# Kernel tuning notes

Hardware: AMD Instinct MI355X
Metric: run time of the kernel (lower is better)

## Reference

```python
import jax, jax.numpy as jnp
import numpy as np

N_CLASSES = 16
REG = 0.1


def setup_inputs() -> dict:
    key = jax.random.key(0)
    k1, k2, k3, k4 = jax.random.split(key, 4)
    N, M, d = 4096, 4096, 1024
    X = jax.random.normal(k1, (N, d), dtype=jnp.float32)
    y = jax.random.randint(k2, (N,), 0, N_CLASSES)
    Xq = jax.random.normal(k3, (M, d), dtype=jnp.float32)
    m = 0.01 * jax.random.normal(k4, (1, d), dtype=jnp.float32)
    kappa = jnp.asarray(0.1, dtype=jnp.float32)
    nu = jnp.asarray(float(d), dtype=jnp.float32)
    triu_diag = jnp.ones((d,), dtype=jnp.float32)
    triu_lower = jnp.eye(d, dtype=jnp.float32) + 0.01 * jax.random.normal(
        jax.random.fold_in(key, 7), (d, d), dtype=jnp.float32)
    return {"X": X, "y": y, "Xq": Xq, "m": m, "kappa": kappa, "nu": nu,
            "triu_diag": triu_diag, "triu_lower": triu_lower}


def reference(X, y, Xq, m, kappa, nu, triu_diag, triu_lower):
    d = X.shape[1]
    C = N_CLASSES
    # Cholesky-factor prior scale: diag(|triu_diag|) + strictly-lower part of triu_lower
    strict_lower = jnp.tril(jnp.ones((d, d), dtype=X.dtype), -1)
    L = jnp.diag(jnp.abs(triu_diag)) + triu_lower * strict_lower
    kap = jnp.abs(kappa) + 1e-6
    nu_ = jnp.maximum(nu, d - 1 + 1e-6)

    # --- fit (vectorized over classes) ---
    onehot = jax.nn.one_hot(y, C, dtype=X.dtype)          # [N, C]
    Nj = onehot.sum(axis=0)                               # [C]
    sums = onehot.T @ X                                   # [C, d] grouped sums
    means = sums / Nj[:, None]                            # [C, d]
    mu = (kap / (kap + Nj))[:, None] * m + (Nj / (kap + Nj))[:, None] * means  # [C, d]
    # grouped scatter: S[c] = X_c^T X_c, via class-weighted features
    Xw = X[:, None, :] * onehot[:, :, None]               # [N, C, d]
    S = jnp.einsum('ncd,ne->cde', Xw, X)                  # [C, d, d]
    base = L @ L.T + kap * (m.T @ m)                      # [d, d]
    sigma = (base[None] + S
             - (kap + Nj)[:, None, None] * jnp.einsum('cd,ce->cde', mu, mu))
    sigma = sigma / (nu_ + Nj + d + 2)[:, None, None]     # [C, d, d]
    eye = jnp.eye(d, dtype=X.dtype)
    sigma_inv = (1.0 - REG) * jnp.linalg.inv(sigma) + REG * eye[None]

    # --- predict: negative Mahalanobis quadratic form per (query, class) ---
    diff = Xq[:, None, :] - mu[None]                      # [M, C, d]
    logits = -jnp.einsum('mcd,cde,mce->mc', diff, sigma_inv, diff)  # [M, C]
    return logits
```

## Files before the change

kernel.cpp:

```cpp
#include <hip/hip_runtime.h>
#include <math.h>

#define DD 1024
#define NP 5120
#define PT_TILES 80
#define TS 65

typedef _Float16 half8 __attribute__((ext_vector_type(8)));
typedef _Float16 half4 __attribute__((ext_vector_type(4)));
typedef float floatx4 __attribute__((ext_vector_type(4)));
typedef short s16x8 __attribute__((ext_vector_type(8)));

#define OFF_XTH   ((size_t)0)
#define OFF_XTL   ((size_t)2621440)
#define OFF_BASE  ((size_t)5242880)
#define OFF_SIGMA ((size_t)6291456)
#define OFF_DINV  ((size_t)23068672)
#define OFF_SUMS  ((size_t)24117248)
#define OFF_MU    ((size_t)24133632)
#define OFF_U     ((size_t)24150016)
#define OFF_MU2   ((size_t)24166400)
#define OFF_XQ2   ((size_t)24166416)
#define OFF_XQMU  ((size_t)24170512)
#define OFF_KAPNU ((size_t)24236048)
#define OFF_CF    ((size_t)24236056)
#define OFF_BETA  ((size_t)24236072)
#define OFF_INVS  ((size_t)24236088)
#define OFF_INTS  ((size_t)24236104)

#define UT_CLS_STRIDE ((size_t)557056)

__device__ __forceinline__ void tri_decode(int b, int& ti, int& tj) {
  int t = 0;
  while ((t + 1) * (t + 2) / 2 <= b) t++;
  ti = t;
  tj = b - t * (t + 1) / 2;
}

__device__ __forceinline__ short f2bf(float f) {
  union { float f; unsigned u; } v; v.f = f;
  unsigned r = v.u + 0x7FFF + ((v.u >> 16) & 1);
  return (short)(r >> 16);
}
__device__ __forceinline__ float bf2f(short b) {
  union { unsigned u; float f; } v; v.u = ((unsigned)(unsigned short)b) << 16; return v.f;
}

__device__ __forceinline__ float reduce256(float v, float* scratch) {
  for (int o = 32; o > 0; o >>= 1) v += __shfl_down(v, o, 64);
  int lane = threadIdx.x & 63, w = threadIdx.x >> 6;
  __syncthreads();
  if (lane == 0) scratch[w] = v;
  __syncthreads();
  return scratch[0] + scratch[1] + scratch[2] + scratch[3];
}

__global__ void k_scalars(const int* y, const float* kappa, const float* nu,
                          float* kapnu, float* cf, float* beta, float* invs,
                          int* counts, int* offsets, int* cls_of_pt, int* order,
                          float* sums, float* uarr, float* dout) {
  __shared__ int h[16];
  __shared__ int cur[16];
  int t = threadIdx.x;
  if (t < 16) h[t] = 0;
  __syncthreads();
  for (int n = t; n < 4096; n += 256) atomicAdd(&h[y[n]], 1);
  __syncthreads();
  if (t == 0) {
    float kap = fabsf(kappa[0]) + 1e-6f;
    float nu_ = fmaxf(nu[0], 1024.0f - 1.0f + 1e-6f);
    kapnu[0] = kap; kapnu[1] = nu_;
    int off = 0, tile = 0;
    for (int c = 0; c < 16; c++) {
      counts[c] = h[c]; offsets[c] = off; cur[c] = off;
      cf[c] = (float)h[c];
      beta[c] = kap + (float)h[c];
      invs[c] = 1.0f / (nu_ + (float)h[c] + 1024.0f + 2.0f);
      int ntile = ((h[c] + 63) & ~63) >> 6;
      for (int q = 0; q < ntile && tile < PT_TILES; q++) cls_of_pt[tile++] = c;
      off += (h[c] + 63) & ~63;
    }
    while (tile < PT_TILES) cls_of_pt[tile++] = -1;
  }
  for (int i = t; i < NP; i += 256) order[i] = -1;
  for (int i = t; i < 16 * 1024; i += 256) { sums[i] = 0.f; uarr[i] = 0.f; }
  for (int i = t; i < 4096 * 16; i += 256) dout[i] = 0.f;
  __syncthreads();
  for (int n = t; n < 4096; n += 256) {
    int c = y[n];
    int p = atomicAdd(&cur[c], 1);
    order[p] = n;
  }
}

__global__ void k_gatherT(const float* X, const int* order, const int* cls_of_pt,
                          short* XTh, short* XTl, float* sums) {
  int pt = blockIdx.x, dt = blockIdx.y, t = threadIdx.x;
  __shared__ float T[64 * TS];
  __shared__ float CS[4 * 64];
  __shared__ int src[64];
  if (t < 64) src[t] = order[pt * 64 + t];
  __syncthreads();
  for (int i = 0; i < 4; i++) {
    int idx4 = i * 256 + t;
    int r = idx4 >> 4, c4 = (idx4 & 15) << 2;
    int s = src[r];
    float4 v = (s >= 0) ? *(const float4*)&X[(size_t)s * DD + dt * 64 + c4]
                        : make_float4(0.f, 0.f, 0.f, 0.f);
    T[r * TS + c4] = v.x; T[r * TS + c4 + 1] = v.y;
    T[r * TS + c4 + 2] = v.z; T[r * TS + c4 + 3] = v.w;
  }
  __syncthreads();
  for (int i = 0; i < 16; i++) {
    int lin = i * 256 + t;
    int d = lin >> 6, p = lin & 63;
    float v = T[p * TS + d];
    short hi = f2bf(v);
    float lov = v - bf2f(hi);
    size_t addr = (size_t)(dt * 64 + d) * NP + pt * 64 + p;
    XTh[addr] = hi;
    XTl[addr] = f2bf(lov);
  }
  int cls = cls_of_pt[pt];
  if (cls < 0) return;
  int g = t >> 6, d = t & 63;
  float s = 0.f;
  for (int p = g * 16; p < g * 16 + 16; p++) s += T[p * TS + d];
  CS[g * 64 + d] = s;
  __syncthreads();
  if (g == 0)
    atomicAdd(&sums[(size_t)cls * DD + dt * 64 + d],
              CS[d] + CS[64 + d] + CS[128 + d] + CS[192 + d]);
}

__global__ void k_mumu2(const float* sums, const float* m, const float* kapnu,
                        const float* cf, float* mu, float* mu2) {
  __shared__ float scratch[4];
  int c = blockIdx.x, t = threadIdx.x;
  float kap = kapnu[0];
  float denom = 1.0f / (kap + cf[c]);
  float s2 = 0.f;
  for (int j = t; j < DD; j += 256) {
    float v = (kap * m[j] + sums[(size_t)c * DD + j]) * denom;
    mu[(size_t)c * DD + j] = v;
    s2 += v * v;
  }
  float tot = reduce256(s2, scratch);
  if (t == 0) mu2[c] = tot;
}

__device__ __forceinline__ float lval(const float* td, const float* tl, int i, int j) {
  if (i == j) return fabsf(td[i]);
  if (i > j) return tl[(size_t)i * DD + j];
  return 0.f;
}

__global__ void k_base(const float* td, const float* tl, const float* m,
                       const float* kapnu, float* base) {
  int ti, tj; tri_decode(blockIdx.x, ti, tj);
  __shared__ float Ta[16][65], Tb[16][65];
  int t = threadIdx.x, tx = t & 15, ty = t >> 4;
  int r0 = ty * 4, c0 = tx * 4;
  float acc[4][4] = {};
  int kmax = (tj + 1) * 64;
  for (int kk = 0; kk < kmax; kk += 16) {
    __syncthreads();
    for (int idx = t; idx < 64 * 16; idx += 256) {
      int r = idx >> 4, p = idx & 15;
      Ta[p][r] = lval(td, tl, ti * 64 + r, kk + p);
      Tb[p][r] = lval(td, tl, tj * 64 + r, kk + p);
    }
    __syncthreads();
#pragma unroll
    for (int p = 0; p < 16; p++) {
      float av[4], bv[4];
#pragma unroll
      for (int a = 0; a < 4; a++) av[a] = Ta[p][r0 + a];
#pragma unroll
      for (int b = 0; b < 4; b++) bv[b] = Tb[p][c0 + b];
#pragma unroll
      for (int a = 0; a < 4; a++)
#pragma unroll
        for (int b = 0; b < 4; b++) acc[a][b] += av[a] * bv[b];
    }
  }
  float kap = kapnu[0];
#pragma unroll
  for (int a = 0; a < 4; a++)
#pragma unroll
    for (int b = 0; b < 4; b++) {
      int gi = ti * 64 + r0 + a, gj = tj * 64 + c0 + b;
      base[(size_t)gi * DD + gj] = acc[a][b] + kap * m[gi] * m[gj];
    }
}

__global__ __launch_bounds__(256) void k_syrk_mfma(const short* XTh, const short* XTl,
                                                   const float* base, const float* mu,
                                                   const float* beta, const float* invs,
                                                   const int* counts, const int* offsets,
                                                   float* sigma) {
  int bb = blockIdx.x;
  int cls = bb / 36, tr = bb % 36;
  int ti, tj; tri_decode(tr, ti, tj);
  int cnt = counts[cls], off = offsets[cls];
  float* Sg = sigma + ((size_t)cls << 20);
  const float* muc = mu + (size_t)cls * DD;
  __shared__ short Ah[128 * 40], Al[128 * 40], Bh[128 * 40], Bl[128 * 40];
  int t = threadIdx.x;
  int wave = t >> 6, lane = t & 63;
  int wr = wave >> 1, wc = wave & 1;
  int quad = lane >> 4, l15 = lane & 15;
  int i0 = ti * 128, j0 = tj * 128;
  bool same = (ti == tj);
  floatx4 acc[4][4];
#pragma unroll
  for (int a = 0; a < 4; a++)
#pragma unroll
    for (int b = 0; b < 4; b++) acc[a][b] = (floatx4){0.f, 0.f, 0.f, 0.f};
  for (int nn = 0; nn < cnt; nn += 32) {
    __syncthreads();
#pragma unroll
    for (int r = 0; r < 2; r++) {
      int lin = r * 256 + t;
      int row = lin >> 2, kg = (lin & 3) << 3;
      size_t sA = (size_t)(i0 + row) * NP + off + nn + kg;
      *(s16x8*)&Ah[row * 40 + kg] = *(const s16x8*)&XTh[sA];
      *(s16x8*)&Al[row * 40 + kg] = *(const s16x8*)&XTl[sA];
      if (!same) {
        size_t sB = (size_t)(j0 + row) * NP + off + nn + kg;
        *(s16x8*)&Bh[row * 40 + kg] = *(const s16x8*)&XTh[sB];
        *(s16x8*)&Bl[row * 40 + kg] = *(const s16x8*)&XTl[sB];
      }
    }
    __syncthreads();
    const short* PBh = same ? Ah : Bh;
    const short* PBl = same ? Al : Bl;
    s16x8 ah[4], al[4], bh[4], bl[4];
#pragma unroll
    for (int f = 0; f < 4; f++) {
      ah[f] = *(const s16x8*)&Ah[(wr * 64 + f * 16 + l15) * 40 + quad * 8];
      al[f] = *(const s16x8*)&Al[(wr * 64 + f * 16 + l15) * 40 + quad * 8];
      bh[f] = *(const s16x8*)&PBh[(wc * 64 + f * 16 + l15) * 40 + quad * 8];
      bl[f] = *(const s16x8*)&PBl[(wc * 64 + f * 16 + l15) * 40 + quad * 8];
    }
#pragma unroll
    for (int fi = 0; fi < 4; fi++)
#pragma unroll
      for (int fj = 0; fj < 4; fj++) {
        acc[fi][fj] = __builtin_amdgcn_mfma_f32_16x16x32_bf16(ah[fi], bh[fj], acc[fi][fj], 0, 0, 0);
        acc[fi][fj] = __builtin_amdgcn_mfma_f32_16x16x32_bf16(ah[fi], bl[fj], acc[fi][fj], 0, 0, 0);
        acc[fi][fj] = __builtin_amdgcn_mfma_f32_16x16x32_bf16(al[fi], bh[fj], acc[fi][fj], 0, 0, 0);
      }
  }
  float bet = beta[cls], isc = invs[cls];
#pragma unroll
  for (int fi = 0; fi < 4; fi++)
#pragma unroll
    for (int fj = 0; fj < 4; fj++)
#pragma unroll
      for (int reg = 0; reg < 4; reg++) {
        int gi = i0 + wr * 64 + fi * 16 + quad * 4 + reg;
        int gj = j0 + wc * 64 + fj * 16 + l15;
        float v = acc[fi][fj][reg] + base[(size_t)gi * DD + gj] - bet * muc[gi] * muc[gj];
        Sg[(size_t)gi * DD + gj] = v * isc;
      }
}

__device__ void chol_inv_reg(float areg[4][4], float* Dinv, int cls, int k, int t,
                             float* Asc, float* Wsc, float* Tsc) {
  __shared__ float colbuf[2][64];
  __shared__ float sdiag[64];
  int tx = t & 15, ty = t >> 4;
  int r0 = ty * 4, c0 = tx * 4;
  for (int j = 0; j < 63; j++) {
    float* cb = colbuf[j & 1];
    if (tx == (j >> 2)) {
      int jj = j & 3;
      cb[r0 + 0] = areg[0][jj];
      cb[r0 + 1] = areg[1][jj];
      cb[r0 + 2] = areg[2][jj];
      cb[r0 + 3] = areg[3][jj];
    }
    __syncthreads();
    float rd = 1.0f / cb[j];
    float rv[4], cv[4];
#pragma unroll
    for (int i = 0; i < 4; i++) rv[i] = cb[r0 + i];
#pragma unroll
    for (int b = 0; b < 4; b++) cv[b] = cb[c0 + b];
#pragma unroll
    for (int i = 0; i < 4; i++)
#pragma unroll
      for (int b = 0; b < 4; b++)
        if (c0 + b > j && c0 + b <= r0 + i)
          areg[i][b] -= rv[i] * cv[b] * rd;
  }
  __syncthreads();
  if (tx == ty) {
#pragma unroll
    for (int i = 0; i < 4; i++) sdiag[r0 + i] = 1.0f / sqrtf(areg[i][i]);
  }
  __syncthreads();
  float sd[4];
#pragma unroll
  for (int b = 0; b < 4; b++) sd[b] = sdiag[c0 + b];
#pragma unroll
  for (int i = 0; i < 4; i++)
#pragma unroll
    for (int b = 0; b < 4; b++) {
      float lv = (r0 + i >= c0 + b) ? areg[i][b] * sd[b] : 0.f;
      Asc[(r0 + i) * TS + c0 + b] = lv;
      Wsc[(r0 + i) * TS + c0 + b] = 0.f;
    }
  __syncthreads();
  if (t < 16) {
    int c = t * 4;
    float l[4][4], w[4][4];
#pragma unroll
    for (int i = 0; i < 4; i++)
#pragma unroll
      for (int j = 0; j <= i; j++) l[i][j] = Asc[(c + i) * TS + c + j];
#pragma unroll
    for (int j = 0; j < 4; j++) {
      w[j][j] = 1.0f / l[j][j];
#pragma unroll
      for (int i = j + 1; i < 4; i++) {
        float s = 0.f;
#pragma unroll
        for (int kk = j; kk < i; kk++) s += l[i][kk] * w[kk][j];
        w[i][j] = -s / l[i][i];
      }
    }
#pragma unroll
    for (int i = 0; i < 4; i++)
#pragma unroll
      for (int j = 0; j <= i; j++) Wsc[(c + i) * TS + c + j] = w[i][j];
  }
  __syncthreads();
#pragma unroll 4
  for (int h = 4; h <= 32; h <<= 1) {
    int hh = h * h;
    int total = 32 * h;
    for (int idx = t; idx < total; idx += 256) {
      int pr = idx / hh;
      int rem = idx - pr * hh;
      int i = rem / h, j = rem - (rem / h) * h;
      int c = pr * 2 * h;
      float s = 0.f;
      for (int kk = j; kk < h; kk++)
        s += Asc[(c + h + i) * TS + c + kk] * Wsc[(c + kk) * TS + c + j];
      Tsc[idx] = s;
    }
    __syncthreads();
    for (int idx = t; idx < total; idx += 256) {
      int pr = idx / hh;
      int rem = idx - pr * hh;
      int i = rem / h, j = rem - (rem / h) * h;
      int c = pr * 2 * h;
      int tb = pr * hh;
      float s = 0.f;
      for (int kk = 0; kk <= i; kk++)
        s += Wsc[(c + h + i) * TS + c + h + kk] * Tsc[tb + kk * h + j];
      Wsc[(c + h + i) * TS + c + j] = -s;
    }
    __syncthreads();
  }
  float* Dv = Dinv + ((size_t)(cls * 16 + k)) * 4096;
  for (int idx4 = t; idx4 < 1024; idx4 += 256) {
    int r = idx4 >> 4, c4 = (idx4 & 15) << 2;
    float4 v = make_float4(Wsc[r * TS + c4], Wsc[r * TS + c4 + 1],
                           Wsc[r * TS + c4 + 2], Wsc[r * TS + c4 + 3]);
    *(float4*)&Dv[r * 64 + c4] = v;
  }
}

__global__ void k_diag0(float* sigma, float* Dinv) {
  __shared__ float A[64 * TS], W[64 * TS];
  __shared__ float Tq[1024];
  int cls = blockIdx.x, t = threadIdx.x;
  int tx = t & 15, ty = t >> 4;
  int r0 = ty * 4, c0 = tx * 4;
  float* Sg = sigma + ((size_t)cls << 20);
  float areg[4][4];
#pragma unroll
  for (int i = 0; i < 4; i++) {
    float4 s = *(const float4*)&Sg[(size_t)(r0 + i) * DD + c0];
    areg[i][0] = s.x; areg[i][1] = s.y; areg[i][2] = s.z; areg[i][3] = s.w;
  }
  chol_inv_reg(areg, Dinv, cls, 0, t, A, W, Tq);
}

__global__ void k_panel(float* sigma, const float* Dinv, int k) {
  __shared__ float B0[64 * TS], B1[64 * TS];
  int i_ = blockIdx.x, cls = blockIdx.y, t = threadIdx.x;
  int tx = t & 15, ty = t >> 4;
  int r0 = ty * 4, c0 = tx * 4;
  int it = k + 1 + i_;
  float* Sg = sigma + ((size_t)cls << 20);
  const float* Dv = Dinv + ((size_t)(cls * 16 + k)) * 4096;
  for (int i = 0; i < 4; i++) {
    int idx4 = i * 256 + t;
    int r = idx4 >> 4, c4 = (idx4 & 15) << 2;
    float4 v0 = *(const float4*)&Dv[r * 64 + c4];
    B0[r * TS + c4] = v0.x; B0[r * TS + c4 + 1] = v0.y;
    B0[r * TS + c4 + 2] = v0.z; B0[r * TS + c4 + 3] = v0.w;
    float4 v1 = *(const float4*)&Sg[(size_t)(it * 64 + r) * DD + k * 64 + c4];
    B1[r * TS + c4] = v1.x; B1[r * TS + c4 + 1] = v1.y;
    B1[r * TS + c4 + 2] = v1.z; B1[r * TS + c4 + 3] = v1.w;
  }
  __syncthreads();
  float a1[4][4] = {};
#pragma unroll 8
  for (int p = 0; p < 64; p++) {
    float bv[4], av1[4];
#pragma unroll
    for (int bq = 0; bq < 4; bq++) bv[bq] = B0[(c0 + bq) * TS + p];
#pragma unroll
    for (int a = 0; a < 4; a++) av1[a] = B1[(r0 + a) * TS + p];
#pragma unroll
    for (int a = 0; a < 4; a++)
#pragma unroll
      for (int bq = 0; bq < 4; bq++) a1[a][bq] += av1[a] * bv[bq];
  }
#pragma unroll
  for (int a = 0; a < 4; a++) {
    float4 v = make_float4(a1[a][0], a1[a][1], a1[a][2], a1[a][3]);
    *(float4*)&Sg[(size_t)(k * 64 + r0 + a) * DD + it * 64 + c0] = v;
  }
}

__global__ void k_update(float* sigma, float* Dinv, int k) {
  __shared__ float B0[64 * TS], B1[64 * TS], B2[64 * TS];
  int b = blockIdx.x, t = threadIdx.x;
  int tx = t & 15, ty = t >> 4;
  int r0 = ty * 4, c0 = tx * 4;
  int nb = 15 - k;
  int nt = nb * (nb + 1) / 2;
  int cls, a_, b_;
  bool special = (b < 16);
  if (special) { cls = b; a_ = 0; b_ = 0; }
  else {
    int jp = b - 16;
    cls = jp / (nt - 1);
    int s = jp % (nt - 1) + 1;
    tri_decode(s, a_, b_);
  }
  int it = k + 1 + a_, jt = k + 1 + b_;
  bool same = (it == jt);
  float* Sg = sigma + ((size_t)cls << 20);
  for (int i = 0; i < 4; i++) {
    int idx4 = i * 256 + t;
    int r = idx4 >> 4, c4 = (idx4 & 15) << 2;
    float4 v1 = *(const float4*)&Sg[(size_t)(k * 64 + r) * DD + it * 64 + c4];
    B1[r * TS + c4] = v1.x; B1[r * TS + c4 + 1] = v1.y;
    B1[r * TS + c4 + 2] = v1.z; B1[r * TS + c4 + 3] = v1.w;
    if (!same) {
      float4 v2 = *(const float4*)&Sg[(size_t)(k * 64 + r) * DD + jt * 64 + c4];
      B2[r * TS + c4] = v2.x; B2[r * TS + c4 + 1] = v2.y;
      B2[r * TS + c4 + 2] = v2.z; B2[r * TS + c4 + 3] = v2.w;
    }
  }
  __syncthreads();
  float* PB = same ? B1 : B2;
  float a3[4][4] = {};
#pragma unroll 8
  for (int p = 0; p < 64; p++) {
    float av[4], bv[4];
#pragma unroll
    for (int a = 0; a < 4; a++) av[a] = B1[(r0 + a) * TS + p];
#pragma unroll
    for (int bq = 0; bq < 4; bq++) bv[bq] = PB[(c0 + bq) * TS + p];
#pragma unroll
    for (int a = 0; a < 4; a++)
#pragma unroll
      for (int bq = 0; bq < 4; bq++) a3[a][bq] += av[a] * bv[bq];
  }
  if (!special) {
#pragma unroll
    for (int a = 0; a < 4; a++) {
      size_t addr = (size_t)(it * 64 + r0 + a) * DD + jt * 64 + c0;
      float4 s = *(const float4*)&Sg[addr];
      s.x -= a3[a][0]; s.y -= a3[a][1]; s.z -= a3[a][2]; s.w -= a3[a][3];
      *(float4*)&Sg[addr] = s;
    }
    return;
  }
  float areg[4][4];
#pragma unroll
  for (int i = 0; i < 4; i++) {
    size_t addr = (size_t)(it * 64 + r0 + i) * DD + jt * 64 + c0;
    float4 s = *(const float4*)&Sg[addr];
    areg[i][0] = s.x - a3[i][0]; areg[i][1] = s.y - a3[i][1];
    areg[i][2] = s.z - a3[i][2]; areg[i][3] = s.w - a3[i][3];
  }
  __syncthreads();
  chol_inv_reg(areg, Dinv, cls, k + 1, t, B1, B2, B0);
}

__global__ void k_cholstep(float* sigma, float* Dinv, int k) {
  __shared__ float B0[64 * TS], B1[64 * TS], B2[64 * TS];
  int b = blockIdx.x, t = threadIdx.x;
  int tx = t & 15, ty = t >> 4;
  int r0 = ty * 4, c0 = tx * 4;
  int nb = 15 - k;
  int nt = nb * (nb + 1) / 2;
  int cls, a_, b_;
  bool special = (b < 16);
  if (special) { cls = b; a_ = 0; b_ = 0; }
  else {
    int jp = b - 16;
    cls = jp / (nt - 1);
    int s = jp % (nt - 1) + 1;
    tri_decode(s, a_, b_);
  }
  int it = k + 1 + a_, jt = k + 1 + b_;
  bool same = (it == jt);
  float* Sg = sigma + ((size_t)cls << 20);
  const float* Dv = Dinv + ((size_t)(cls * 16 + k)) * 4096;
  for (int i = 0; i < 4; i++) {
    int idx4 = i * 256 + t;
    int r = idx4 >> 4, c4 = (idx4 & 15) << 2;
    float4 v0 = *(const float4*)&Dv[r * 64 + c4];
    B0[r * TS + c4] = v0.x; B0[r * TS + c4 + 1] = v0.y;
    B0[r * TS + c4 + 2] = v0.z; B0[r * TS + c4 + 3] = v0.w;
    float4 v1 = *(const float4*)&Sg[(size_t)(it * 64 + r) * DD + k * 64 + c4];
    B1[r * TS + c4] = v1.x; B1[r * TS + c4 + 1] = v1.y;
    B1[r * TS + c4 + 2] = v1.z; B1[r * TS + c4 + 3] = v1.w;
    if (!same) {
      float4 v2 = *(const float4*)&Sg[(size_t)(jt * 64 + r) * DD + k * 64 + c4];
      B2[r * TS + c4] = v2.x; B2[r * TS + c4 + 1] = v2.y;
      B2[r * TS + c4 + 2] = v2.z; B2[r * TS + c4 + 3] = v2.w;
    }
  }
  __syncthreads();
  float a1[4][4] = {}, a2[4][4] = {};
#pragma unroll 8
  for (int p = 0; p < 64; p++) {
    float bv[4], av1[4];
#pragma unroll
    for (int bq = 0; bq < 4; bq++) bv[bq] = B0[(c0 + bq) * TS + p];
#pragma unroll
    for (int a = 0; a < 4; a++) av1[a] = B1[(r0 + a) * TS + p];
#pragma unroll
    for (int a = 0; a < 4; a++)
#pragma unroll
      for (int bq = 0; bq < 4; bq++) a1[a][bq] += av1[a] * bv[bq];
    if (!same) {
      float av2[4];
#pragma unroll
      for (int a = 0; a < 4; a++) av2[a] = B2[(r0 + a) * TS + p];
#pragma unroll
      for (int a = 0; a < 4; a++)
#pragma unroll
        for (int bq = 0; bq < 4; bq++) a2[a][bq] += av2[a] * bv[bq];
    }
  }
  __syncthreads();
#pragma unroll
  for (int a = 0; a < 4; a++)
#pragma unroll
    for (int bq = 0; bq < 4; bq++) {
      B1[(r0 + a) * TS + c0 + bq] = a1[a][bq];
      if (!same) B2[(r0 + a) * TS + c0 + bq] = a2[a][bq];
    }
  if (b_ == 0) {
#pragma unroll
    for (int a = 0; a < 4; a++) {
      float4 v = make_float4(a1[a][0], a1[a][1], a1[a][2], a1[a][3]);
      *(float4*)&Sg[(size_t)(k * 64 + r0 + a) * DD + it * 64 + c0] = v;
    }
  }
  __syncthreads();
  float* PB = same ? B1 : B2;
  float a3[4][4] = {};
#pragma unroll 8
  for (int p = 0; p < 64; p++) {
    float av[4], bv[4];
#pragma unroll
    for (int a = 0; a < 4; a++) av[a] = B1[(r0 + a) * TS + p];
#pragma unroll
    for (int bq = 0; bq < 4; bq++) bv[bq] = PB[(c0 + bq) * TS + p];
#pragma unroll
    for (int a = 0; a < 4; a++)
#pragma unroll
      for (int bq = 0; bq < 4; bq++) a3[a][bq] += av[a] * bv[bq];
  }
  if (!special) {
#pragma unroll
    for (int a = 0; a < 4; a++) {
      size_t addr = (size_t)(it * 64 + r0 + a) * DD + jt * 64 + c0;
      float4 s = *(const float4*)&Sg[addr];
      s.x -= a3[a][0]; s.y -= a3[a][1]; s.z -= a3[a][2]; s.w -= a3[a][3];
      *(float4*)&Sg[addr] = s;
    }
    return;
  }
  float areg[4][4];
#pragma unroll
  for (int i = 0; i < 4; i++) {
    size_t addr = (size_t)(it * 64 + r0 + i) * DD + jt * 64 + c0;
    float4 s = *(const float4*)&Sg[addr];
    areg[i][0] = s.x - a3[i][0]; areg[i][1] = s.y - a3[i][1];
    areg[i][2] = s.z - a3[i][2]; areg[i][3] = s.w - a3[i][3];
  }
  __syncthreads();
  chol_inv_reg(areg, Dinv, cls, k + 1, t, B1, B2, B0);
}

__global__ void k_vl1(float* sigma, const float* Dinv) {
  __shared__ float Rl[64 * TS], W0s[64 * TS], W1s[64 * TS], Ts[64 * TS];
  int b = blockIdx.x, t = threadIdx.x;
  int cls = b >> 3, i = b & 7;
  int t0 = 2 * i, t1 = 2 * i + 1;
  float* Sg = sigma + ((size_t)cls << 20);
  int tx = t & 15, ty = t >> 4;
  int r0 = ty * 4, c0 = tx * 4;
  const float* Dv0 = Dinv + ((size_t)(cls * 16 + t0)) * 4096;
  const float* Dv1 = Dinv + ((size_t)(cls * 16 + t1)) * 4096;
  for (int idx4 = t; idx4 < 1024; idx4 += 256) {
    int r = idx4 >> 4, c4 = (idx4 & 15) << 2;
    float4 vr = *(const float4*)&Sg[(size_t)(t0 * 64 + r) * DD + t1 * 64 + c4];
    Rl[r * TS + c4] = vr.x; Rl[r * TS + c4 + 1] = vr.y;
    Rl[r * TS + c4 + 2] = vr.z; Rl[r * TS + c4 + 3] = vr.w;
    float4 v0 = *(const float4*)&Dv0[r * 64 + c4];
    W0s[r * TS + c4] = v0.x; W0s[r * TS + c4 + 1] = v0.y;
    W0s[r * TS + c4 + 2] = v0.z; W0s[r * TS + c4 + 3] = v0.w;
    float4 v1 = *(const float4*)&Dv1[r * 64 + c4];
    W1s[r * TS + c4] = v1.x; W1s[r * TS + c4 + 1] = v1.y;
    W1s[r * TS + c4 + 2] = v1.z; W1s[r * TS + c4 + 3] = v1.w;
  }
  __syncthreads();
  float aT[4][4] = {};
#pragma unroll 8
  for (int p = 0; p < 64; p++) {
    float av[4], bv[4];
#pragma unroll
    for (int a = 0; a < 4; a++) av[a] = Rl[(r0 + a) * TS + p];
#pragma unroll
    for (int bq = 0; bq < 4; bq++) bv[bq] = W0s[p * TS + c0 + bq];
#pragma unroll
    for (int a = 0; a < 4; a++)
#pragma unroll
      for (int bq = 0; bq < 4; bq++) aT[a][bq] += av[a] * bv[bq];
  }
  __syncthreads();
#pragma unroll
  for (int a = 0; a < 4; a++)
#pragma unroll
    for (int bq = 0; bq < 4; bq++) Ts[(r0 + a) * TS + c0 + bq] = aT[a][bq];
  __syncthreads();
  float aV[4][4] = {};
#pragma unroll 8
  for (int p = 0; p < 64; p++) {
    float av[4], bv[4];
#pragma unroll
    for (int a = 0; a < 4; a++) av[a] = W1s[(r0 + a) * TS + p];
#pragma unroll
    for (int bq = 0; bq < 4; bq++) bv[bq] = Ts[p * TS + c0 + bq];
#pragma unroll
    for (int a = 0; a < 4; a++)
#pragma unroll
      for (int bq = 0; bq < 4; bq++) aV[a][bq] += av[a] * bv[bq];
  }
#pragma unroll
  for (int a = 0; a < 4; a++)
    *(float4*)&Sg[(size_t)(t0 * 64 + r0 + a) * DD + t1 * 64 + c0] =
        make_float4(-aV[a][0], -aV[a][1], -aV[a][2], -aV[a][3]);
}

__global__ void k_vlA(float* sigma, const float* Dinv, int w) {
  __shared__ float Xs[64 * TS], Ys[64 * TS];
  int aa = blockIdx.x / w, bb = blockIdx.x % w;
  int base = blockIdx.y * 2 * w, cls = blockIdx.z;
  float* Sg = sigma + ((size_t)cls << 20);
  int t = threadIdx.x, tx = t & 15, ty = t >> 4;
  int r0 = ty * 4, c0 = tx * 4;
  float acc[4][4] = {};
  for (int m = bb; m < w; m++) {
    __syncthreads();
    for (int idx4 = t; idx4 < 1024; idx4 += 256) {
      int r = idx4 >> 4, c4 = (idx4 & 15) << 2;
      float4 v = *(const float4*)&Sg[(size_t)((base + m) * 64 + r) * DD + (base + w + aa) * 64 + c4];
      Xs[r * TS + c4] = v.x; Xs[r * TS + c4 + 1] = v.y;
      Xs[r * TS + c4 + 2] = v.z; Xs[r * TS + c4 + 3] = v.w;
    }
    if (m == bb) {
      const float* Dv = Dinv + ((size_t)(cls * 16 + base + bb)) * 4096;
      for (int idx4 = t; idx4 < 1024; idx4 += 256) {
        int r = idx4 >> 4, c4 = (idx4 & 15) << 2;
        float4 v = *(const float4*)&Dv[r * 64 + c4];
        Ys[r * TS + c4] = v.x; Ys[r * TS + c4 + 1] = v.y;
        Ys[r * TS + c4 + 2] = v.z; Ys[r * TS + c4 + 3] = v.w;
      }
    } else {
      for (int idx4 = t; idx4 < 1024; idx4 += 256) {
        int p = idx4 >> 4, c4 = (idx4 & 15) << 2;
        float4 v = *(const float4*)&Sg[(size_t)((base + bb) * 64 + p) * DD + (base + m) * 64 + c4];
        Ys[p * TS + c4] = v.x; Ys[p * TS + c4 + 1] = v.y;
        Ys[p * TS + c4 + 2] = v.z; Ys[p * TS + c4 + 3] = v.w;
      }
    }
    __syncthreads();
#pragma unroll 8
    for (int p = 0; p < 64; p++) {
      float av[4], bv[4];
#pragma unroll
      for (int a = 0; a < 4; a++) av[a] = Xs[(r0 + a) * TS + p];
#pragma unroll
      for (int bq = 0; bq < 4; bq++) bv[bq] = Ys[p * TS + c0 + bq];
#pragma unroll
      for (int a = 0; a < 4; a++)
#pragma unroll
        for (int bq = 0; bq < 4; bq++) acc[a][bq] += av[a] * bv[bq];
    }
  }
#pragma unroll
  for (int a = 0; a < 4; a++)
    *(float4*)&Sg[(size_t)((base + w + aa) * 64 + r0 + a) * DD + (base + bb) * 64 + c0] =
        make_float4(acc[a][0], acc[a][1], acc[a][2], acc[a][3]);
}

__global__ void k_vlB(float* sigma, const float* Dinv, int w) {
  __shared__ float Xs[64 * TS], Ys[64 * TS];
  int aa = blockIdx.x / w, bb = blockIdx.x % w;
  int base = blockIdx.y * 2 * w, cls = blockIdx.z;
  float* Sg = sigma + ((size_t)cls << 20);
  int t = threadIdx.x, tx = t & 15, ty = t >> 4;
  int r0 = ty * 4, c0 = tx * 4;
  float acc[4][4] = {};
  for (int m = 0; m <= aa; m++) {
    __syncthreads();
    if (m == aa) {
      const float* Dv = Dinv + ((size_t)(cls * 16 + base + w + aa)) * 4096;
      for (int idx4 = t; idx4 < 1024; idx4 += 256) {
        int r = idx4 >> 4, c4 = (idx4 & 15) << 2;
        float4 v = *(const float4*)&Dv[r * 64 + c4];
        Xs[r * TS + c4] = v.x; Xs[r * TS + c4 + 1] = v.y;
        Xs[r * TS + c4 + 2] = v.z; Xs[r * TS + c4 + 3] = v.w;
      }
    } else {
      for (int idx4 = t; idx4 < 1024; idx4 += 256) {
        int r = idx4 >> 4, c4 = (idx4 & 15) << 2;
        float4 v = *(const float4*)&Sg[(size_t)((base + w + m) * 64 + r) * DD + (base + w + aa) * 64 + c4];
        Xs[r * TS + c4] = v.x; Xs[r * TS + c4 + 1] = v.y;
        Xs[r * TS + c4 + 2] = v.z; Xs[r * TS + c4 + 3] = v.w;
      }
    }
    for (int idx4 = t; idx4 < 1024; idx4 += 256) {
      int p = idx4 >> 4, c4 = (idx4 & 15) << 2;
      float4 v = *(const float4*)&Sg[(size_t)((base + w + m) * 64 + p) * DD + (base + bb) * 64 + c4];
      Ys[p * TS + c4] = v.x; Ys[p * TS + c4 + 1] = v.y;
      Ys[p * TS + c4 + 2] = v.z; Ys[p * TS + c4 + 3] = v.w;
    }
    __syncthreads();
#pragma unroll 8
    for (int p = 0; p < 64; p++) {
      float av[4], bv[4];
#pragma unroll
      for (int a = 0; a < 4; a++) av[a] = Xs[(r0 + a) * TS + p];
#pragma unroll
      for (int bq = 0; bq < 4; bq++) bv[bq] = Ys[p * TS + c0 + bq];
#pragma unroll
      for (int a = 0; a < 4; a++)
#pragma unroll
        for (int bq = 0; bq < 4; bq++) acc[a][bq] += av[a] * bv[bq];
    }
  }
#pragma unroll
  for (int a = 0; a < 4; a++)
    *(float4*)&Sg[(size_t)((base + bb) * 64 + r0 + a) * DD + (base + w + aa) * 64 + c0] =
        make_float4(-acc[a][0], -acc[a][1], -acc[a][2], -acc[a][3]);
}

__global__ void k_finalize(const float* sigma, const float* Dinv, const float* mu,
                           float* uarr, _Float16* UT) {
  __shared__ float U0[64 * TS];
  __shared__ float CS[4 * 64];
  int jp = blockIdx.x, t = threadIdx.x;
  int cls = jp / 136, tr = jp % 136;
  int nt_, kt_; tri_decode(tr, nt_, kt_);
  const float* muc = mu + (size_t)cls * DD;
  _Float16* outp = UT + (size_t)cls * UT_CLS_STRIDE + (size_t)tr * 4096;
  const float* srcp;
  size_t row_stride;
  if (kt_ == nt_) {
    srcp = Dinv + ((size_t)(cls * 16 + nt_)) * 4096;
    row_stride = 64;
  } else {
    srcp = sigma + ((size_t)cls << 20) + (size_t)(kt_ * 64) * DD + nt_ * 64;
    row_stride = DD;
  }
  for (int i = 0; i < 2; i++) {
    int g8 = i * 256 + t;
    int rr = g8 >> 3, c8 = (g8 & 7) << 3;
    float4 v0 = *(const float4*)&srcp[(size_t)rr * row_stride + c8];
    float4 v1 = *(const float4*)&srcp[(size_t)rr * row_stride + c8 + 4];
    half8 h;
    h[0] = (_Float16)v0.x; h[1] = (_Float16)v0.y; h[2] = (_Float16)v0.z; h[3] = (_Float16)v0.w;
    h[4] = (_Float16)v1.x; h[5] = (_Float16)v1.y; h[6] = (_Float16)v1.z; h[7] = (_Float16)v1.w;
    *(half8*)&outp[rr * 64 + c8] = h;
    U0[rr * TS + c8] = v0.x; U0[rr * TS + c8 + 1] = v0.y;
    U0[rr * TS + c8 + 2] = v0.z; U0[rr * TS + c8 + 3] = v0.w;
    U0[rr * TS + c8 + 4] = v1.x; U0[rr * TS + c8 + 5] = v1.y;
    U0[rr * TS + c8 + 6] = v1.z; U0[rr * TS + c8 + 7] = v1.w;
  }
  __syncthreads();
  int g = t >> 6, r = t & 63;
  float s = 0.f;
  for (int c = g * 16; c < g * 16 + 16; c++)
    s += U0[r * TS + c] * muc[kt_ * 64 + c];
  CS[g * 64 + r] = s;
  __syncthreads();
  if (g == 0)
    atomicAdd(&uarr[(size_t)cls * DD + nt_ * 64 + r],
              CS[r] + CS[64 + r] + CS[128 + r] + CS[192 + r]);
}

__global__ void k_xqdots(const float* Xq, const float* mu, float* xq2, float* xqmu,
                         _Float16* XqH) {
  __shared__ float xrow[DD];
  int m = blockIdx.x, t = threadIdx.x;
  for (int i = t; i < 256; i += 256)
    ((float4*)xrow)[i] = ((const float4*)(Xq + (size_t)m * DD))[i];
  __syncthreads();
  for (int i = t; i < 256; i += 256) {
    float4 v = ((const float4*)xrow)[i];
    half4 h = {(_Float16)v.x, (_Float16)v.y, (_Float16)v.z, (_Float16)v.w};
    *(half4*)&XqH[(size_t)m * DD + i * 4] = h;
  }
  int wave = t >> 6, lane = t & 63;
  for (int cc = 0; cc < 4; cc++) {
    int c = wave * 4 + cc;
    const float* muc = mu + (size_t)c * DD;
    float s = 0.f;
    for (int j = lane; j < DD; j += 64) s += xrow[j] * muc[j];
    for (int o = 32; o > 0; o >>= 1) s += __shfl_down(s, o, 64);
    if (lane == 0) xqmu[(size_t)m * 16 + c] = s;
  }
  if (wave == 0) {
    float s = 0.f;
    for (int j = lane; j < DD; j += 64) s += xrow[j] * xrow[j];
    for (int o = 32; o > 0; o >>= 1) s += __shfl_down(s, o, 64);
    if (lane == 0) xq2[m] = s;
  }
}

__global__ __launch_bounds__(256) void k_gemmG_mfma(const _Float16* XqH, const _Float16* UT,
                                                    const float* u, float* dout) {
  int mt = blockIdx.x, ct = blockIdx.y, cls = blockIdx.z;
  const _Float16* Uc = UT + (size_t)cls * UT_CLS_STRIDE;
  __shared__ _Float16 As[128 * 40];
  __shared__ _Float16 Bs[128 * 40];
  int t = threadIdx.x;
  int wave = t >> 6, lane = t & 63;
  int wr = wave >> 1, wc = wave & 1;
  int quad = lane >> 4, l15 = lane & 15;
  int m0 = mt * 128, n0 = ct * 128, NT0 = ct * 2;
  floatx4 acc[4][4];
#pragma unroll
  for (int a = 0; a < 4; a++)
#pragma unroll
    for (int b = 0; b < 4; b++) acc[a][b] = (floatx4){0.f, 0.f, 0.f, 0.f};
  int kmax = (ct + 1) * 128;
  for (int kk = 0; kk < kmax; kk += 32) {
    __syncthreads();
#pragma unroll
    for (int i = 0; i < 2; i++) {
      int lin = i * 256 + t;
      int r = lin >> 2, kg = (lin & 3) * 8;
      *(half8*)&As[r * 40 + kg] = *(const half8*)&XqH[(size_t)(m0 + r) * DD + kk + kg];
    }
    int kt = kk >> 6, k0 = kk & 63;
#pragma unroll
    for (int i = 0; i < 2; i++) {
      int lin = i * 256 + t;
      int nl = lin >> 2, kg = (lin & 3) * 8;
      int s = nl >> 6, np = nl & 63;
      int nt = NT0 + s;
      half8 v = {};
      if (kt <= nt)
        v = *(const half8*)&Uc[(size_t)(nt * (nt + 1) / 2 + kt) * 4096 + np * 64 + k0 + kg];
      *(half8*)&Bs[nl * 40 + kg] = v;
    }
    __syncthreads();
    half8 af[4], bf[4];
#pragma unroll
    for (int f = 0; f < 4; f++) {
      af[f] = *(const half8*)&As[(wr * 64 + f * 16 + l15) * 40 + quad * 8];
      bf[f] = *(const half8*)&Bs[(wc * 64 + f * 16 + l15) * 40 + quad * 8];
    }
#pragma unroll
    for (int fi = 0; fi < 4; fi++)
#pragma unroll
      for (int fj = 0; fj < 4; fj++)
        acc[fi][fj] = __builtin_amdgcn_mfma_f32_16x16x32_f16(af[fi], bf[fj], acc[fi][fj], 0, 0, 0);
  }
  float uv[4];
#pragma unroll
  for (int fj = 0; fj < 4; fj++)
    uv[fj] = u[(size_t)cls * DD + n0 + wc * 64 + fj * 16 + l15];
#pragma unroll
  for (int fi = 0; fi < 4; fi++) {
#pragma unroll
    for (int r = 0; r < 4; r++) {
      float p = 0.f;
#pragma unroll
      for (int fj = 0; fj < 4; fj++) {
        float e = acc[fi][fj][r] - uv[fj];
        p += e * e;
      }
      p += __shfl_xor(p, 1, 64);
      p += __shfl_xor(p, 2, 64);
      p += __shfl_xor(p, 4, 64);
      p += __shfl_xor(p, 8, 64);
      if (l15 == 0) {
        int m = m0 + wr * 64 + fi * 16 + quad * 4 + r;
        atomicAdd(&dout[(size_t)m * 16 + cls], p);
      }
    }
  }
}

__global__ void k_logits(const float* xq2, const float* xqmu, const float* mu2,
                         float* dout) {
  size_t idx = (size_t)blockIdx.x * 256 + threadIdx.x;
  int m = (int)(idx >> 4), c = (int)(idx & 15);
  float q1 = dout[idx];
  float q2 = xq2[m] - 2.0f * xqmu[idx] + mu2[c];
  dout[idx] = -(0.9f * q1 + 0.1f * q2);
}

extern "C" void kernel_launch(void* const* d_in, const int* in_sizes, int n_in,
                              void* d_out, int out_size, void* d_ws, size_t ws_size,
                              hipStream_t stream) {
  (void)in_sizes; (void)n_in; (void)out_size; (void)ws_size;
  const float* X  = (const float*)d_in[0];
  const int*   y  = (const int*)d_in[1];
  const float* Xq = (const float*)d_in[2];
  const float* m  = (const float*)d_in[3];
  const float* kappa = (const float*)d_in[4];
  const float* nu = (const float*)d_in[5];
  const float* td = (const float*)d_in[6];
  const float* tl = (const float*)d_in[7];
  float* out = (float*)d_out;
  float* ws = (float*)d_ws;

  short* XTh   = (short*)(ws + OFF_XTH);
  short* XTl   = (short*)(ws + OFF_XTL);
  _Float16* UT = (_Float16*)ws;
  float* baseb = ws + OFF_BASE;
  float* sigma = ws + OFF_SIGMA;
  _Float16* XqH = (_Float16*)sigma;
  float* Dinv  = ws + OFF_DINV;
  float* sums  = ws + OFF_SUMS;
  float* mu    = ws + OFF_MU;
  float* uarr  = ws + OFF_U;
  float* mu2   = ws + OFF_MU2;
  float* xq2   = ws + OFF_XQ2;
  float* xqmu  = ws + OFF_XQMU;
  float* kapnu = ws + OFF_KAPNU;
  float* cf    = ws + OFF_CF;
  float* beta  = ws + OFF_BETA;
  float* invs  = ws + OFF_INVS;
  int* ints      = (int*)(ws + OFF_INTS);
  int* counts    = ints;
  int* offsets   = ints + 16;
  int* cls_of_pt = ints + 32;
  int* order     = ints + 32 + PT_TILES;

  k_scalars<<<1, 256, 0, stream>>>(y, kappa, nu, kapnu, cf, beta, invs,
                                   counts, offsets, cls_of_pt, order,
                                   sums, uarr, out);
  k_gatherT<<<dim3(PT_TILES, 16), 256, 0, stream>>>(X, order, cls_of_pt, XTh, XTl, sums);
  k_mumu2<<<16, 256, 0, stream>>>(sums, m, kapnu, cf, mu, mu2);
  k_base<<<136, 256, 0, stream>>>(td, tl, m, kapnu, baseb);
  k_syrk_mfma<<<16 * 36, 256, 0, stream>>>(XTh, XTl, baseb, mu, beta, invs,
                                           counts, offsets, sigma);
  k_diag0<<<16, 256, 0, stream>>>(sigma, Dinv);
  for (int k = 0; k < 15; k++) {
    int nb = 15 - k;
    int nt = nb * (nb + 1) / 2;
    if (k <= 7) {
      k_panel<<<dim3(nb, 16), 256, 0, stream>>>(sigma, Dinv, k);
      k_update<<<16 * nt, 256, 0, stream>>>(sigma, Dinv, k);
    } else {
      k_cholstep<<<16 * nt, 256, 0, stream>>>(sigma, Dinv, k);
    }
  }
  k_vl1<<<128, 256, 0, stream>>>(sigma, Dinv);
  for (int L = 2; L <= 4; L++) {
    int w = 1 << (L - 1);
    int ncomb = 8 >> (L - 1);
    k_vlA<<<dim3(w * w, ncomb, 16), 256, 0, stream>>>(sigma, Dinv, w);
    k_vlB<<<dim3(w * w, ncomb, 16), 256, 0, stream>>>(sigma, Dinv, w);
  }
  k_finalize<<<16 * 136, 256, 0, stream>>>(sigma, Dinv, mu, uarr, UT);
  k_xqdots<<<4096, 256, 0, stream>>>(Xq, mu, xq2, xqmu, XqH);
  k_gemmG_mfma<<<dim3(32, 8, 16), 256, 0, stream>>>(XqH, UT, uarr, out);
  k_logits<<<256, 256, 0, stream>>>(xq2, xqmu, mu2, out);
}
```

Measured before the change: 1.488 ms.

## Block the 64x64 diagonal Cholesky into 4-wide panels to cut barriers

Replaces the column-by-column right-looking Cholesky of each 64x64 diagonal tile, which needed 63 block barriers, with a blocked version over 4x4 register tiles. Each of the 16 steps factors a 4x4 diagonal block redundantly in every thread, solves the panel, and applies a rank-4 update. This removes most __syncthreads and the separate diagonal-scaling pass, at the cost of redundant per-thread small-block factorization and a different rounding order.

```diff
diff --git a/kernel.cpp b/kernel.cpp
--- a/kernel.cpp
+++ b/kernel.cpp
@@ -268,47 +268,85 @@
 
 __device__ void chol_inv_reg(float areg[4][4], float* Dinv, int cls, int k, int t,
                              float* Asc, float* Wsc, float* Tsc) {
-  __shared__ float colbuf[2][64];
-  __shared__ float sdiag[64];
+  __shared__ float Pn[2][64 * 5];
   int tx = t & 15, ty = t >> 4;
   int r0 = ty * 4, c0 = tx * 4;
-  for (int j = 0; j < 63; j++) {
-    float* cb = colbuf[j & 1];
-    if (tx == (j >> 2)) {
-      int jj = j & 3;
-      cb[r0 + 0] = areg[0][jj];
-      cb[r0 + 1] = areg[1][jj];
-      cb[r0 + 2] = areg[2][jj];
-      cb[r0 + 3] = areg[3][jj];
-    }
-    __syncthreads();
-    float rd = 1.0f / cb[j];
-    float rv[4], cv[4];
-#pragma unroll
-    for (int i = 0; i < 4; i++) rv[i] = cb[r0 + i];
-#pragma unroll
-    for (int b = 0; b < 4; b++) cv[b] = cb[c0 + b];
-#pragma unroll
-    for (int i = 0; i < 4; i++)
-#pragma unroll
-      for (int b = 0; b < 4; b++)
-        if (c0 + b > j && c0 + b <= r0 + i)
-          areg[i][b] -= rv[i] * cv[b] * rd;
-  }
-  __syncthreads();
-  if (tx == ty) {
-#pragma unroll
-    for (int i = 0; i < 4; i++) sdiag[r0 + i] = 1.0f / sqrtf(areg[i][i]);
-  }
-  __syncthreads();
-  float sd[4];
-#pragma unroll
-  for (int b = 0; b < 4; b++) sd[b] = sdiag[c0 + b];
+  for (int jb = 0; jb < 16; jb++) {
+    float* P = Pn[jb & 1];
+    if (tx == jb) {
+#pragma unroll
+      for (int i = 0; i < 4; i++)
+#pragma unroll
+        for (int b = 0; b < 4; b++) P[(r0 + i) * 5 + b] = areg[i][b];
+    }
+    __syncthreads();
+    if (tx >= jb) {
+      int cb = jb * 4;
+      float d00 = P[(cb + 0) * 5 + 0];
+      float d10 = P[(cb + 1) * 5 + 0], d11 = P[(cb + 1) * 5 + 1];
+      float d20 = P[(cb + 2) * 5 + 0], d21 = P[(cb + 2) * 5 + 1], d22 = P[(cb + 2) * 5 + 2];
+      float d30 = P[(cb + 3) * 5 + 0], d31 = P[(cb + 3) * 5 + 1], d32 = P[(cb + 3) * 5 + 2], d33 = P[(cb + 3) * 5 + 3];
+      float L00 = sqrtf(d00), i00 = 1.0f / L00;
+      float l10 = d10 * i00, l20 = d20 * i00, l30 = d30 * i00;
+      float L11 = sqrtf(d11 - l10 * l10), i11 = 1.0f / L11;
+      float l21 = (d21 - l20 * l10) * i11;
+      float l31 = (d31 - l30 * l10) * i11;
+      float L22 = sqrtf(d22 - l20 * l20 - l21 * l21), i22 = 1.0f / L22;
+      float l32 = (d32 - l30 * l20 - l31 * l21) * i22;
+      float L33 = sqrtf(d33 - l30 * l30 - l31 * l31 - l32 * l32);
+      if (ty == jb) {
+        if (tx == jb) {
+          areg[0][0] = L00; areg[0][1] = 0.f; areg[0][2] = 0.f; areg[0][3] = 0.f;
+          areg[1][0] = l10; areg[1][1] = L11; areg[1][2] = 0.f; areg[1][3] = 0.f;
+          areg[2][0] = l20; areg[2][1] = l21; areg[2][2] = L22; areg[2][3] = 0.f;
+          areg[3][0] = l30; areg[3][1] = l31; areg[3][2] = l32; areg[3][3] = L33;
+        }
+      } else if (ty > jb) {
+        float i33 = 1.0f / L33;
+        float Wr[4][4];
+#pragma unroll
+        for (int i = 0; i < 4; i++) {
+          float b0 = P[(r0 + i) * 5 + 0], b1 = P[(r0 + i) * 5 + 1];
+          float b2 = P[(r0 + i) * 5 + 2], b3 = P[(r0 + i) * 5 + 3];
+          float w0 = b0 * i00;
+          float w1 = (b1 - w0 * l10) * i11;
+          float w2 = (b2 - w0 * l20 - w1 * l21) * i22;
+          float w3 = (b3 - w0 * l30 - w1 * l31 - w2 * l32) * i33;
+          Wr[i][0] = w0; Wr[i][1] = w1; Wr[i][2] = w2; Wr[i][3] = w3;
+        }
+        if (tx == jb) {
+#pragma unroll
+          for (int i = 0; i < 4; i++)
+#pragma unroll
+            for (int b = 0; b < 4; b++) areg[i][b] = Wr[i][b];
+        } else if (ty >= tx) {
+          float Wc[4][4];
+#pragma unroll
+          for (int b = 0; b < 4; b++) {
+            float b0 = P[(c0 + b) * 5 + 0], b1 = P[(c0 + b) * 5 + 1];
+            float b2 = P[(c0 + b) * 5 + 2], b3 = P[(c0 + b) * 5 + 3];
+            float w0 = b0 * i00;
+            float w1 = (b1 - w0 * l10) * i11;
+            float w2 = (b2 - w0 * l20 - w1 * l21) * i22;
+            float w3 = (b3 - w0 * l30 - w1 * l31 - w2 * l32) * i33;
+            Wc[b][0] = w0; Wc[b][1] = w1; Wc[b][2] = w2; Wc[b][3] = w3;
+          }
+#pragma unroll
+          for (int i = 0; i < 4; i++)
+#pragma unroll
+            for (int b = 0; b < 4; b++)
+              if (r0 + i >= c0 + b)
+                areg[i][b] -= Wr[i][0] * Wc[b][0] + Wr[i][1] * Wc[b][1]
+                            + Wr[i][2] * Wc[b][2] + Wr[i][3] * Wc[b][3];
+        }
+      }
+    }
+  }
 #pragma unroll
   for (int i = 0; i < 4; i++)
 #pragma unroll
     for (int b = 0; b < 4; b++) {
-      float lv = (r0 + i >= c0 + b) ? areg[i][b] * sd[b] : 0.f;
+      float lv = (r0 + i >= c0 + b) ? areg[i][b] : 0.f;
       Asc[(r0 + i) * TS + c0 + b] = lv;
       Wsc[(r0 + i) * TS + c0 + b] = 0.f;
     }
```

Measured after the change: 1.518 ms. +2.1%, slower.

## Use direct global-to-LDS loads in predict GEMM and skip masked triangular tiles

Applied to the files above, without the earlier changes.

The predict GEMM now stages A and B tiles with global_load_lds (direct global-to-LDS DMA) instead of loading into registers and storing to shared memory. Padding is dropped so rows are 32 halves wide. Waves whose B half lies entirely beyond the triangular band skip their MFMA work, and column tiles are launched in reverse so the longest blocks start first. The unpadded layout may add LDS bank conflicts on fragment reads, and the zero-fill for out-of-band B tiles is gone, so correctness depends on the skip condition exactly matching the old masked region.

```diff
diff --git a/kernel.cpp b/kernel.cpp
--- a/kernel.cpp
+++ b/kernel.cpp
@@ -847,15 +847,23 @@
 
 __global__ __launch_bounds__(256) void k_gemmG_mfma(const _Float16* XqH, const _Float16* UT,
                                                     const float* u, float* dout) {
-  int mt = blockIdx.x, ct = blockIdx.y, cls = blockIdx.z;
+  int mt = blockIdx.x, ct = 7 - (int)blockIdx.y, cls = blockIdx.z;
   const _Float16* Uc = UT + (size_t)cls * UT_CLS_STRIDE;
-  __shared__ _Float16 As[128 * 40];
-  __shared__ _Float16 Bs[128 * 40];
+  __shared__ _Float16 As[128 * 32];
+  __shared__ _Float16 Bs[128 * 32];
   int t = threadIdx.x;
   int wave = t >> 6, lane = t & 63;
   int wr = wave >> 1, wc = wave & 1;
   int quad = lane >> 4, l15 = lane & 15;
   int m0 = mt * 128, n0 = ct * 128, NT0 = ct * 2;
+  int lin1 = 256 + t;
+  int r0_ = t >> 2, kg0 = (t & 3) * 8;
+  int r1_ = lin1 >> 2, kg1 = (lin1 & 3) * 8;
+  int s0_ = r0_ >> 6, np0 = r0_ & 63;
+  int s1_ = r1_ >> 6, np1 = r1_ & 63;
+  int nt0_ = NT0 + s0_, nt1_ = NT0 + s1_;
+  size_t btile0 = (size_t)(nt0_ * (nt0_ + 1) / 2) * 4096 + (size_t)np0 * 64 + kg0;
+  size_t btile1 = (size_t)(nt1_ * (nt1_ + 1) / 2) * 4096 + (size_t)np1 * 64 + kg1;
   floatx4 acc[4][4];
 #pragma unroll
   for (int a = 0; a < 4; a++)
@@ -864,36 +872,33 @@
   int kmax = (ct + 1) * 128;
   for (int kk = 0; kk < kmax; kk += 32) {
     __syncthreads();
-#pragma unroll
-    for (int i = 0; i < 2; i++) {
-      int lin = i * 256 + t;
-      int r = lin >> 2, kg = (lin & 3) * 8;
-      *(half8*)&As[r * 40 + kg] = *(const half8*)&XqH[(size_t)(m0 + r) * DD + kk + kg];
-    }
     int kt = kk >> 6, k0 = kk & 63;
-#pragma unroll
-    for (int i = 0; i < 2; i++) {
-      int lin = i * 256 + t;
-      int nl = lin >> 2, kg = (lin & 3) * 8;
-      int s = nl >> 6, np = nl & 63;
-      int nt = NT0 + s;
-      half8 v = {};
-      if (kt <= nt)
-        v = *(const half8*)&Uc[(size_t)(nt * (nt + 1) / 2 + kt) * 4096 + np * 64 + k0 + kg];
-      *(half8*)&Bs[nl * 40 + kg] = v;
-    }
-    __syncthreads();
-    half8 af[4], bf[4];
-#pragma unroll
-    for (int f = 0; f < 4; f++) {
-      af[f] = *(const half8*)&As[(wr * 64 + f * 16 + l15) * 40 + quad * 8];
-      bf[f] = *(const half8*)&Bs[(wc * 64 + f * 16 + l15) * 40 + quad * 8];
-    }
-#pragma unroll
-    for (int fi = 0; fi < 4; fi++)
-#pragma unroll
-      for (int fj = 0; fj < 4; fj++)
-        acc[fi][fj] = __builtin_amdgcn_mfma_f32_16x16x32_f16(af[fi], bf[fj], acc[fi][fj], 0, 0, 0);
+    __builtin_amdgcn_global_load_lds(
+        (const __attribute__((address_space(1))) uint32_t*)&XqH[(size_t)(m0 + r0_) * DD + kk + kg0],
+        (__attribute__((address_space(3))) uint32_t*)&As[(size_t)t * 8], 16, 0, 0);
+    __builtin_amdgcn_global_load_lds(
+        (const __attribute__((address_space(1))) uint32_t*)&XqH[(size_t)(m0 + r1_) * DD + kk + kg1],
+        (__attribute__((address_space(3))) uint32_t*)&As[(size_t)lin1 * 8], 16, 0, 0);
+    __builtin_amdgcn_global_load_lds(
+        (const __attribute__((address_space(1))) uint32_t*)&Uc[btile0 + (size_t)kt * 4096 + k0],
+        (__attribute__((address_space(3))) uint32_t*)&Bs[(size_t)t * 8], 16, 0, 0);
+    __builtin_amdgcn_global_load_lds(
+        (const __attribute__((address_space(1))) uint32_t*)&Uc[btile1 + (size_t)kt * 4096 + k0],
+        (__attribute__((address_space(3))) uint32_t*)&Bs[(size_t)lin1 * 8], 16, 0, 0);
+    __syncthreads();
+    if (!(wc == 0 && kt > NT0)) {
+      half8 af[4], bf[4];
+#pragma unroll
+      for (int f = 0; f < 4; f++) {
+        af[f] = *(const half8*)&As[(wr * 64 + f * 16 + l15) * 32 + quad * 8];
+        bf[f] = *(const half8*)&Bs[(wc * 64 + f * 16 + l15) * 32 + quad * 8];
+      }
+#pragma unroll
+      for (int fi = 0; fi < 4; fi++)
+#pragma unroll
+        for (int fj = 0; fj < 4; fj++)
+          acc[fi][fj] = __builtin_amdgcn_mfma_f32_16x16x32_f16(af[fi], bf[fj], acc[fi][fj], 0, 0, 0);
+    }
   }
   float uv[4];
 #pragma unroll
```

New measurement: 1.489 ms. Within noise of the previous version (+0.1%).

## Factor 64x64 diagonal Cholesky block in a single wavefront using shuffles

Applied to the files above, without the earlier changes.

Replaces the 63-step right-looking Cholesky of the diagonal block, which needed a block-wide barrier per column, with a single-wavefront factorization. Each of 64 lanes owns one column in registers and broadcasts pivot values via __shfl. The remaining three waves zero the workspace in parallel. This removes per-column __syncthreads and shared-memory traffic, at the cost of 64-float register arrays per lane and serialized shuffle work.

```diff
diff --git a/kernel.cpp b/kernel.cpp
--- a/kernel.cpp
+++ b/kernel.cpp
@@ -268,50 +268,47 @@
 
 __device__ void chol_inv_reg(float areg[4][4], float* Dinv, int cls, int k, int t,
                              float* Asc, float* Wsc, float* Tsc) {
-  __shared__ float colbuf[2][64];
-  __shared__ float sdiag[64];
   int tx = t & 15, ty = t >> 4;
   int r0 = ty * 4, c0 = tx * 4;
-  for (int j = 0; j < 63; j++) {
-    float* cb = colbuf[j & 1];
-    if (tx == (j >> 2)) {
-      int jj = j & 3;
-      cb[r0 + 0] = areg[0][jj];
-      cb[r0 + 1] = areg[1][jj];
-      cb[r0 + 2] = areg[2][jj];
-      cb[r0 + 3] = areg[3][jj];
-    }
-    __syncthreads();
-    float rd = 1.0f / cb[j];
-    float rv[4], cv[4];
-#pragma unroll
-    for (int i = 0; i < 4; i++) rv[i] = cb[r0 + i];
-#pragma unroll
-    for (int b = 0; b < 4; b++) cv[b] = cb[c0 + b];
-#pragma unroll
-    for (int i = 0; i < 4; i++)
-#pragma unroll
-      for (int b = 0; b < 4; b++)
-        if (c0 + b > j && c0 + b <= r0 + i)
-          areg[i][b] -= rv[i] * cv[b] * rd;
-  }
-  __syncthreads();
-  if (tx == ty) {
-#pragma unroll
-    for (int i = 0; i < 4; i++) sdiag[r0 + i] = 1.0f / sqrtf(areg[i][i]);
-  }
-  __syncthreads();
-  float sd[4];
-#pragma unroll
-  for (int b = 0; b < 4; b++) sd[b] = sdiag[c0 + b];
 #pragma unroll
   for (int i = 0; i < 4; i++)
 #pragma unroll
-    for (int b = 0; b < 4; b++) {
-      float lv = (r0 + i >= c0 + b) ? areg[i][b] * sd[b] : 0.f;
-      Asc[(r0 + i) * TS + c0 + b] = lv;
-      Wsc[(r0 + i) * TS + c0 + b] = 0.f;
-    }
+    for (int b = 0; b < 4; b++)
+      Asc[(r0 + i) * TS + c0 + b] = areg[i][b];
+  __syncthreads();
+  if (t < 64) {
+    int c = t;
+    float a[64];
+#pragma unroll
+    for (int i = 0; i < 64; i++) a[i] = Asc[i * TS + c];
+    float rd = 0.f;
+#pragma unroll
+    for (int jb = 0; jb < 8; jb++) {
+      for (int jo = 0; jo < 8; jo++) {
+        int j = jb * 8 + jo;
+        float se = 0.f;
+#pragma unroll
+        for (int i = jb * 8; i < 64; i++) {
+          float u = __shfl(a[i], j, 64);
+          if (i == j) rd = 1.0f / u;
+          se = (i == c && c > j) ? u * rd : se;
+          a[i] -= u * se;
+        }
+      }
+    }
+    float dval = 1.f;
+#pragma unroll
+    for (int i = 0; i < 64; i++) dval = (i == c) ? a[i] : dval;
+    float sd = 1.0f / sqrtf(dval);
+#pragma unroll
+    for (int i = 0; i < 64; i++)
+      Asc[i * TS + c] = (i >= c) ? a[i] * sd : 0.f;
+  } else {
+    for (int idx = t - 64; idx < 4096; idx += 192) {
+      int r = idx >> 6, cz = idx & 63;
+      Wsc[r * TS + cz] = 0.f;
+    }
+  }
   __syncthreads();
   if (t < 16) {
     int c = t * 4;
```

New measurement: 2.715 ms. +82.5%, slower.
